# Performance work log

Hardware: AMD Instinct MI355X
Metric: run time of the kernel (lower is better)

The kernel has to match this reference:

```python
import jax, jax.numpy as jnp
import numpy as np

DT = 1.0
MIN_INFILTRATION = 0.1
EPS = 1e-6


def setup_inputs() -> dict:
    key = jax.random.key(0)
    k1, k2, k3, k4 = jax.random.split(key, 4)
    B, T = 16384, 2048
    # physically plausible scales
    precip = jax.random.uniform(k1, (B, T), dtype=jnp.float32) * 10.0        # mm/hr
    K = jax.random.uniform(k2, (B, 1), dtype=jnp.float32) * 20.0 + 0.5       # mm/hr
    psi = jax.random.uniform(k3, (B, 1), dtype=jnp.float32) * 200.0 + 10.0   # mm
    delta_theta = jax.random.uniform(k4, (B, 1), dtype=jnp.float32) * 0.5    # -
    return {"precip": precip, "K": K, "psi": psi, "delta_theta": delta_theta}


def reference(precip, K, psi, delta_theta):
    # precip: (B, T); K, psi, delta_theta: (B, 1)
    Kv = K[:, 0]
    pd = psi[:, 0] * delta_theta[:, 0]  # psi * delta_theta, (B,)

    def step(F, P_t):
        f_cap = jnp.maximum(Kv * (1.0 + pd / jnp.maximum(F, EPS)), MIN_INFILTRATION)
        f_act = jnp.minimum(P_t, f_cap)
        runoff = jnp.maximum(P_t - f_act, 0.0)
        F_new = F + f_act * DT
        return F_new, (f_act, runoff, F_new)

    F0 = jnp.zeros_like(precip[:, 0])  # (B,)
    _, (infil, runoff, cumF) = jax.lax.scan(step, F0, precip.T)  # (T, B) each
    return infil.T, runoff.T, cumF.T
```

## Files before the change

kernel.cpp:

```cpp
#include <hip/hip_runtime.h>


#define GA_MIN_INF 0.1f
#define GA_EPS 1e-6f

typedef float f4 __attribute__((ext_vector_type(4)));

constexpr int ROWS  = 64;
constexpr int TS    = 64;
constexpr int PITCH = 68;

__global__ __launch_bounds__(448, 1) void ga_pc(
    const float* __restrict__ precip, const float* __restrict__ K,
    const float* __restrict__ psi, const float* __restrict__ dtheta,
    float* __restrict__ out, int B, int T) {
  __shared__ float sb[2][3][ROWS * PITCH];

  const int tid  = threadIdx.x;
  const int wid  = tid >> 6;
  const int lane = tid & 63;
  const int rowbase = blockIdx.x * ROWS;

  const size_t BT = (size_t)B * (size_t)T;
  const int nstage = T / TS;
  const int nsb    = T / 32;

  if (wid == 0) {
    const int b = rowbase + lane;
    const float Kv  = K[b];
    const float kpd = Kv * (psi[b] * dtheta[b]);
    const f4* __restrict__ pr = reinterpret_cast<const f4*>(precip + (size_t)b * T);

    float F = 0.0f;
    f4 buf[8], nxt[8];
#pragma unroll
    for (int i = 0; i < 8; ++i) buf[i] = pr[i];

    int sbc = 0;
    for (int st = 0; st < nstage; ++st) {
      const int pb = st & 1;
      float* const L0 = &sb[pb][0][lane * PITCH];
      float* const L1 = &sb[pb][1][lane * PITCH];
      float* const L2 = &sb[pb][2][lane * PITCH];
#pragma unroll
      for (int q = 0; q < 2; ++q) {
        if (sbc + 1 < nsb) {
#pragma unroll
          for (int i = 0; i < 8; ++i) nxt[i] = pr[(sbc + 1) * 8 + i];
        }
#pragma unroll
        for (int i = 0; i < 8; ++i) {
          const f4 p = buf[i];
          f4 a, r, c;
#pragma unroll
          for (int j = 0; j < 4; ++j) {
            float rF   = __builtin_amdgcn_rcpf(fmaxf(F, GA_EPS));
            float fcap = fmaxf(Kv + kpd * rF, GA_MIN_INF);
            float fact = fminf(p[j], fcap);
            r[j] = fmaxf(p[j] - fact, 0.0f);
            F += fact;
            a[j] = fact;
            c[j] = F;
          }
          const int t0 = q * 32 + i * 4;
          *reinterpret_cast<f4*>(L0 + t0) = a;
          *reinterpret_cast<f4*>(L1 + t0) = r;
          *reinterpret_cast<f4*>(L2 + t0) = c;
        }
#pragma unroll
        for (int i = 0; i < 8; ++i) buf[i] = nxt[i];
        ++sbc;
      }
      asm volatile("s_waitcnt lgkmcnt(0)" ::: "memory");
      __builtin_amdgcn_s_barrier();
    }
  } else {
    const int s = (wid - 1) % 3;
    const int h = (wid - 1) / 3;
    float* const dst = out + (size_t)s * BT;
    const int fr = lane >> 4;
    const int fc = (lane & 15) * 4;

    for (int st = 0; st < nstage; ++st) {
      if (st > 0) {
        const int tb = (st - 1) * TS;
        const float* const src = &sb[(st - 1) & 1][s][0];
#pragma unroll
        for (int g = 0; g < 8; ++g) {
          const int r = h * 32 + g * 4 + fr;
          f4 v = *reinterpret_cast<const f4*>(&src[r * PITCH + fc]);
          __builtin_nontemporal_store(
              v, reinterpret_cast<f4*>(dst + (size_t)(rowbase + r) * T + tb + fc));
        }
      }
      asm volatile("s_waitcnt lgkmcnt(0)" ::: "memory");
      __builtin_amdgcn_s_barrier();
    }
    {
      const int tb = (nstage - 1) * TS;
      const float* const src = &sb[(nstage - 1) & 1][s][0];
#pragma unroll
      for (int g = 0; g < 8; ++g) {
        const int r = h * 32 + g * 4 + fr;
        f4 v = *reinterpret_cast<const f4*>(&src[r * PITCH + fc]);
        __builtin_nontemporal_store(
            v, reinterpret_cast<f4*>(dst + (size_t)(rowbase + r) * T + tb + fc));
      }
    }
  }
}

__global__ void ga_fallback(
    const float* __restrict__ precip, const float* __restrict__ K,
    const float* __restrict__ psi, const float* __restrict__ dtheta,
    float* __restrict__ out, int B, int T) {
  int b = blockIdx.x * blockDim.x + threadIdx.x;
  if (b >= B) return;
  const float Kv  = K[b];
  const float kpd = Kv * (psi[b] * dtheta[b]);
  const size_t BT = (size_t)B * (size_t)T;
  float F = 0.0f;
  for (int t = 0; t < T; ++t) {
    float pv   = precip[(size_t)b * T + t];
    float rF   = __builtin_amdgcn_rcpf(fmaxf(F, GA_EPS));
    float fcap = fmaxf(Kv + kpd * rF, GA_MIN_INF);
    float fact = fminf(pv, fcap);
    float ro   = fmaxf(pv - fact, 0.0f);
    F += fact;
    out[(size_t)b * T + t] = fact;
    out[BT + (size_t)b * T + t] = ro;
    out[2 * BT + (size_t)b * T + t] = F;
  }
}

extern "C" void kernel_launch(void* const* d_in, const int* in_sizes, int n_in,
                              void* d_out, int out_size, void* d_ws, size_t ws_size,
                              hipStream_t stream) {
  const float* precip = (const float*)d_in[0];
  const float* K      = (const float*)d_in[1];
  const float* psi    = (const float*)d_in[2];
  const float* dtheta = (const float*)d_in[3];
  float* out = (float*)d_out;

  const int B = in_sizes[1];
  const int T = in_sizes[0] / B;

  if ((B % ROWS) == 0 && (T % TS) == 0 && ((T / 32) % 2) == 0) {
    ga_pc<<<B / ROWS, 448, 0, stream>>>(precip, K, psi, dtheta, out, B, T);
  } else {
    ga_fallback<<<(B + 63) / 64, 64, 0, stream>>>(precip, K, psi, dtheta, out, B, T);
  }
}
```

Measured before the change: 106.0 us.

## Replace block barriers with LDS flag-based producer/consumer sync and triple buffering

Replaces the per-stage workgroup barrier between the single compute wave and the six store waves with atomic LDS counters. The producer waits only until consumers have drained the buffer it is about to overwrite, and consumers signal release as soon as their LDS reads finish, before issuing global stores. A third shared buffer is added so the producer can run further ahead. This is meant to keep the serial recurrence wave from stalling on slow global stores, at the cost of spin-waiting and more LDS use. It relies on relaxed atomics plus compiler barriers for ordering.

```diff
diff --git a/kernel.cpp b/kernel.cpp
--- a/kernel.cpp
+++ b/kernel.cpp
@@ -9,17 +9,30 @@
 constexpr int ROWS  = 64;
 constexpr int TS    = 64;
 constexpr int PITCH = 68;
+constexpr int DEPTH = 3;
+constexpr int NCONS = 6;
+
+__device__ __forceinline__ void wait_ge(int* p, int v) {
+  while (__hip_atomic_load(p, __ATOMIC_RELAXED, __HIP_MEMORY_SCOPE_WORKGROUP) < v)
+    __builtin_amdgcn_s_sleep(1);
+  asm volatile("" ::: "memory");
+}
 
 __global__ __launch_bounds__(448, 1) void ga_pc(
     const float* __restrict__ precip, const float* __restrict__ K,
     const float* __restrict__ psi, const float* __restrict__ dtheta,
     float* __restrict__ out, int B, int T) {
-  __shared__ float sb[2][3][ROWS * PITCH];
+  __shared__ float sb[DEPTH][3][ROWS * PITCH];
+  __shared__ int prod_stage;
+  __shared__ int done_count;
 
   const int tid  = threadIdx.x;
   const int wid  = tid >> 6;
   const int lane = tid & 63;
   const int rowbase = blockIdx.x * ROWS;
+
+  if (tid == 0) { prod_stage = 0; done_count = 0; }
+  __syncthreads();
 
   const size_t BT = (size_t)B * (size_t)T;
   const int nstage = T / TS;
@@ -38,7 +51,9 @@
 
     int sbc = 0;
     for (int st = 0; st < nstage; ++st) {
-      const int pb = st & 1;
+      wait_ge(&done_count, NCONS * (st - DEPTH + 1));
+
+      const int pb = st % DEPTH;
       float* const L0 = &sb[pb][0][lane * PITCH];
       float* const L1 = &sb[pb][1][lane * PITCH];
       float* const L2 = &sb[pb][2][lane * PITCH];
@@ -72,7 +87,9 @@
         ++sbc;
       }
       asm volatile("s_waitcnt lgkmcnt(0)" ::: "memory");
-      __builtin_amdgcn_s_barrier();
+      if (lane == 0)
+        __hip_atomic_store(&prod_stage, st + 1, __ATOMIC_RELAXED,
+                           __HIP_MEMORY_SCOPE_WORKGROUP);
     }
   } else {
     const int s = (wid - 1) % 3;
@@ -82,29 +99,24 @@
     const int fc = (lane & 15) * 4;
 
     for (int st = 0; st < nstage; ++st) {
-      if (st > 0) {
-        const int tb = (st - 1) * TS;
-        const float* const src = &sb[(st - 1) & 1][s][0];
-#pragma unroll
-        for (int g = 0; g < 8; ++g) {
-          const int r = h * 32 + g * 4 + fr;
-          f4 v = *reinterpret_cast<const f4*>(&src[r * PITCH + fc]);
-          __builtin_nontemporal_store(
-              v, reinterpret_cast<f4*>(dst + (size_t)(rowbase + r) * T + tb + fc));
-        }
-      }
-      asm volatile("s_waitcnt lgkmcnt(0)" ::: "memory");
-      __builtin_amdgcn_s_barrier();
-    }
-    {
-      const int tb = (nstage - 1) * TS;
-      const float* const src = &sb[(nstage - 1) & 1][s][0];
+      wait_ge(&prod_stage, st + 1);
+      const int tb = st * TS;
+      const float* const src = &sb[st % DEPTH][s][0];
+      f4 v[8];
 #pragma unroll
       for (int g = 0; g < 8; ++g) {
         const int r = h * 32 + g * 4 + fr;
-        f4 v = *reinterpret_cast<const f4*>(&src[r * PITCH + fc]);
+        v[g] = *reinterpret_cast<const f4*>(&src[r * PITCH + fc]);
+      }
+      asm volatile("s_waitcnt lgkmcnt(0)" ::: "memory");
+      if (lane == 0)
+        __hip_atomic_fetch_add(&done_count, 1, __ATOMIC_RELAXED,
+                               __HIP_MEMORY_SCOPE_WORKGROUP);
+#pragma unroll
+      for (int g = 0; g < 8; ++g) {
+        const int r = h * 32 + g * 4 + fr;
         __builtin_nontemporal_store(
-            v, reinterpret_cast<f4*>(dst + (size_t)(rowbase + r) * T + tb + fc));
+            v[g], reinterpret_cast<f4*>(dst + (size_t)(rowbase + r) * T + tb + fc));
       }
     }
   }
```

Result: slower. 112.6 us (+6.2%).

## Split scan into checkpoint pass and segment-parallel output pass

Applied to the files above, without the earlier changes.

Adds a first kernel that runs the full recurrence per row without writing outputs and records the cumulative infiltration at 16 segment boundaries into workspace. A second kernel restarts from those checkpoints so 32 lanes handle 2 rows × 16 segments in parallel, staging results through LDS for three store waves. The goal is to shorten the serial dependency chain in the store-producing kernel. The cost is an extra full read of precip, a second launch, and a producer wave that is only half active and loops over all 64 rows of the block.

```diff
diff --git a/kernel.cpp b/kernel.cpp
--- a/kernel.cpp
+++ b/kernel.cpp
@@ -6,105 +6,161 @@
 
 typedef float f4 __attribute__((ext_vector_type(4)));
 
-constexpr int ROWS  = 64;
-constexpr int TS    = 64;
-constexpr int PITCH = 68;
-
-__global__ __launch_bounds__(448, 1) void ga_pc(
+constexpr int SEGS  = 16;
+constexpr int PITCH = 132;
+constexpr int RPI   = 2;
+constexpr int CHUNK = SEGS * PITCH;
+
+__device__ __forceinline__ void ga_step(float& F, float Kv, float kpd,
+                                        float pv, float& fi, float& ro) {
+  float rF   = __builtin_amdgcn_rcpf(fmaxf(F, GA_EPS));
+  float fcap = fmaxf(Kv + kpd * rF, GA_MIN_INF);
+  float fact = fminf(pv, fcap);
+  ro = fmaxf(pv - fact, 0.0f);
+  F += fact;
+  fi = fact;
+}
+
+__global__ __launch_bounds__(64, 1) void ga_pass1(
     const float* __restrict__ precip, const float* __restrict__ K,
     const float* __restrict__ psi, const float* __restrict__ dtheta,
-    float* __restrict__ out, int B, int T) {
-  __shared__ float sb[2][3][ROWS * PITCH];
+    float* __restrict__ cp, int B, int T) {
+  const int b = blockIdx.x * 64 + threadIdx.x;
+  if (b >= B) return;
+  const float Kv  = K[b];
+  const float kpd = Kv * (psi[b] * dtheta[b]);
+  const f4* __restrict__ pr = reinterpret_cast<const f4*>(precip + (size_t)b * T);
+
+  const int nbat = T / 32;
+  const int bats_per_seg = (T / SEGS) / 32;
+
+  float F = 0.0f;
+  f4 buf[8], nxt[8];
+#pragma unroll
+  for (int i = 0; i < 8; ++i) buf[i] = pr[i];
+
+  for (int bat = 0; bat < nbat; ++bat) {
+    if ((bat % bats_per_seg) == 0) cp[(size_t)(bat / bats_per_seg) * B + b] = F;
+    if (bat + 1 < nbat) {
+#pragma unroll
+      for (int i = 0; i < 8; ++i) nxt[i] = pr[(bat + 1) * 8 + i];
+    }
+#pragma unroll
+    for (int i = 0; i < 8; ++i) {
+      const f4 p = buf[i];
+#pragma unroll
+      for (int j = 0; j < 4; ++j) {
+        float fi_, ro_;
+        ga_step(F, Kv, kpd, p[j], fi_, ro_);
+      }
+    }
+#pragma unroll
+    for (int i = 0; i < 8; ++i) buf[i] = nxt[i];
+  }
+}
+
+__global__ __launch_bounds__(256, 1) void ga_pass2(
+    const float* __restrict__ precip, const float* __restrict__ K,
+    const float* __restrict__ psi, const float* __restrict__ dtheta,
+    const float* __restrict__ cp, float* __restrict__ out, int B, int T) {
+  __shared__ float sb[2][3][RPI * CHUNK];
 
   const int tid  = threadIdx.x;
   const int wid  = tid >> 6;
   const int lane = tid & 63;
-  const int rowbase = blockIdx.x * ROWS;
+  const int rowbase = blockIdx.x * 64;
 
   const size_t BT = (size_t)B * (size_t)T;
-  const int nstage = T / TS;
-  const int nsb    = T / 32;
+  const int seglen = T / SEGS;
+  const int niter  = 64 / RPI;
 
   if (wid == 0) {
-    const int b = rowbase + lane;
-    const float Kv  = K[b];
-    const float kpd = Kv * (psi[b] * dtheta[b]);
-    const f4* __restrict__ pr = reinterpret_cast<const f4*>(precip + (size_t)b * T);
-
-    float F = 0.0f;
-    f4 buf[8], nxt[8];
-#pragma unroll
-    for (int i = 0; i < 8; ++i) buf[i] = pr[i];
-
-    int sbc = 0;
-    for (int st = 0; st < nstage; ++st) {
-      const int pb = st & 1;
-      float* const L0 = &sb[pb][0][lane * PITCH];
-      float* const L1 = &sb[pb][1][lane * PITCH];
-      float* const L2 = &sb[pb][2][lane * PITCH];
-#pragma unroll
-      for (int q = 0; q < 2; ++q) {
-        if (sbc + 1 < nsb) {
-#pragma unroll
-          for (int i = 0; i < 8; ++i) nxt[i] = pr[(sbc + 1) * 8 + i];
+    const int row = lane & 1;
+    const int seg = lane >> 1;
+    const bool active = lane < 32;
+
+    for (int it = 0; it < niter; ++it) {
+      const int pb = it & 1;
+      if (active) {
+        const int grow = rowbase + it * RPI + row;
+        const float Kv  = K[grow];
+        const float kpd = Kv * (psi[grow] * dtheta[grow]);
+        float F = cp[(size_t)seg * B + grow];
+        const f4* __restrict__ pr =
+            reinterpret_cast<const f4*>(precip + (size_t)grow * T + seg * seglen);
+        float* const L0 = &sb[pb][0][row * CHUNK + seg * PITCH];
+        float* const L1 = &sb[pb][1][row * CHUNK + seg * PITCH];
+        float* const L2 = &sb[pb][2][row * CHUNK + seg * PITCH];
+
+        f4 buf[8], nxt[8];
+#pragma unroll
+        for (int i = 0; i < 8; ++i) buf[i] = pr[i];
+#pragma unroll
+        for (int q = 0; q < 4; ++q) {
+          if (q < 3) {
+#pragma unroll
+            for (int i = 0; i < 8; ++i) nxt[i] = pr[(q + 1) * 8 + i];
+          }
+#pragma unroll
+          for (int i = 0; i < 8; ++i) {
+            const f4 p = buf[i];
+            f4 a, r, c;
+#pragma unroll
+            for (int j = 0; j < 4; ++j) {
+              float fi_, ro_;
+              ga_step(F, Kv, kpd, p[j], fi_, ro_);
+              a[j] = fi_; r[j] = ro_; c[j] = F;
+            }
+            const int t0 = q * 32 + i * 4;
+            *reinterpret_cast<f4*>(L0 + t0) = a;
+            *reinterpret_cast<f4*>(L1 + t0) = r;
+            *reinterpret_cast<f4*>(L2 + t0) = c;
+          }
+#pragma unroll
+          for (int i = 0; i < 8; ++i) buf[i] = nxt[i];
         }
-#pragma unroll
-        for (int i = 0; i < 8; ++i) {
-          const f4 p = buf[i];
-          f4 a, r, c;
-#pragma unroll
-          for (int j = 0; j < 4; ++j) {
-            float rF   = __builtin_amdgcn_rcpf(fmaxf(F, GA_EPS));
-            float fcap = fmaxf(Kv + kpd * rF, GA_MIN_INF);
-            float fact = fminf(p[j], fcap);
-            r[j] = fmaxf(p[j] - fact, 0.0f);
-            F += fact;
-            a[j] = fact;
-            c[j] = F;
-          }
-          const int t0 = q * 32 + i * 4;
-          *reinterpret_cast<f4*>(L0 + t0) = a;
-          *reinterpret_cast<f4*>(L1 + t0) = r;
-          *reinterpret_cast<f4*>(L2 + t0) = c;
-        }
-#pragma unroll
-        for (int i = 0; i < 8; ++i) buf[i] = nxt[i];
-        ++sbc;
       }
       asm volatile("s_waitcnt lgkmcnt(0)" ::: "memory");
       __builtin_amdgcn_s_barrier();
     }
   } else {
-    const int s = (wid - 1) % 3;
-    const int h = (wid - 1) / 3;
-    float* const dst = out + (size_t)s * BT;
-    const int fr = lane >> 4;
-    const int fc = (lane & 15) * 4;
-
-    for (int st = 0; st < nstage; ++st) {
-      if (st > 0) {
-        const int tb = (st - 1) * TS;
-        const float* const src = &sb[(st - 1) & 1][s][0];
-#pragma unroll
-        for (int g = 0; g < 8; ++g) {
-          const int r = h * 32 + g * 4 + fr;
-          f4 v = *reinterpret_cast<const f4*>(&src[r * PITCH + fc]);
-          __builtin_nontemporal_store(
-              v, reinterpret_cast<f4*>(dst + (size_t)(rowbase + r) * T + tb + fc));
+    const int s = wid - 1;
+    float* const dstS = out + (size_t)s * BT;
+    const int segl = lane >> 5;
+    const int off  = (lane & 31) * 4;
+
+    for (int it = 0; it < niter; ++it) {
+      if (it > 0) {
+        const float* const src = &sb[(it - 1) & 1][s][0];
+#pragma unroll
+        for (int r = 0; r < RPI; ++r) {
+          const int grow = rowbase + (it - 1) * RPI + r;
+          float* const dst = dstS + (size_t)grow * T;
+#pragma unroll
+          for (int g = 0; g < 8; ++g) {
+            const int idx = r * CHUNK + (g * 2 + segl) * PITCH + off;
+            f4 v = *reinterpret_cast<const f4*>(&src[idx]);
+            __builtin_nontemporal_store(
+                v, reinterpret_cast<f4*>(dst + g * 256 + lane * 4));
+          }
         }
       }
       asm volatile("s_waitcnt lgkmcnt(0)" ::: "memory");
       __builtin_amdgcn_s_barrier();
     }
     {
-      const int tb = (nstage - 1) * TS;
-      const float* const src = &sb[(nstage - 1) & 1][s][0];
-#pragma unroll
-      for (int g = 0; g < 8; ++g) {
-        const int r = h * 32 + g * 4 + fr;
-        f4 v = *reinterpret_cast<const f4*>(&src[r * PITCH + fc]);
-        __builtin_nontemporal_store(
-            v, reinterpret_cast<f4*>(dst + (size_t)(rowbase + r) * T + tb + fc));
+      const float* const src = &sb[(niter - 1) & 1][s][0];
+#pragma unroll
+      for (int r = 0; r < RPI; ++r) {
+        const int grow = rowbase + (niter - 1) * RPI + r;
+        float* const dst = dstS + (size_t)grow * T;
+#pragma unroll
+        for (int g = 0; g < 8; ++g) {
+          const int idx = r * CHUNK + (g * 2 + segl) * PITCH + off;
+          f4 v = *reinterpret_cast<const f4*>(&src[idx]);
+          __builtin_nontemporal_store(
+              v, reinterpret_cast<f4*>(dst + g * 256 + lane * 4));
+        }
       }
     }
   }
@@ -121,14 +177,11 @@
   const size_t BT = (size_t)B * (size_t)T;
   float F = 0.0f;
   for (int t = 0; t < T; ++t) {
-    float pv   = precip[(size_t)b * T + t];
-    float rF   = __builtin_amdgcn_rcpf(fmaxf(F, GA_EPS));
-    float fcap = fmaxf(Kv + kpd * rF, GA_MIN_INF);
-    float fact = fminf(pv, fcap);
-    float ro   = fmaxf(pv - fact, 0.0f);
-    F += fact;
-    out[(size_t)b * T + t] = fact;
-    out[BT + (size_t)b * T + t] = ro;
+    float pv = precip[(size_t)b * T + t];
+    float fi_, ro_;
+    ga_step(F, Kv, kpd, pv, fi_, ro_);
+    out[(size_t)b * T + t] = fi_;
+    out[BT + (size_t)b * T + t] = ro_;
     out[2 * BT + (size_t)b * T + t] = F;
   }
 }
@@ -145,8 +198,13 @@
   const int B = in_sizes[1];
   const int T = in_sizes[0] / B;
 
-  if ((B % ROWS) == 0 && (T % TS) == 0 && ((T / 32) % 2) == 0) {
-    ga_pc<<<B / ROWS, 448, 0, stream>>>(precip, K, psi, dtheta, out, B, T);
+  const size_t cp_bytes = (size_t)SEGS * (size_t)B * sizeof(float);
+  const bool ok = (B % 64) == 0 && T == 2048;
+
+  if (ws_size >= cp_bytes && ok) {
+    float* cp = (float*)d_ws;
+    ga_pass1<<<B / 64, 64, 0, stream>>>(precip, K, psi, dtheta, cp, B, T);
+    ga_pass2<<<B / 64, 256, 0, stream>>>(precip, K, psi, dtheta, cp, out, B, T);
   } else {
     ga_fallback<<<(B + 63) / 64, 64, 0, stream>>>(precip, K, psi, dtheta, out, B, T);
   }
```

After: 215.7 us. +103.5%, slower.
